# Kernel tuning notes

Hardware: AMD Instinct MI355X
Metric: run time of the kernel (lower is better)

The kernel has to match this reference:

```python
import jax, jax.numpy as jnp
import numpy as np

C = 512
H_HEADS = 8  # self-attn heads (num_heads) and cross-attn heads (n_heads), both 8


def _self_attn(x, Wq, Wkv):
    # x: [B,N,C]; shared (ModuleParallel) linear weights, qkv_bias=False
    B, N, _ = x.shape
    h, d = H_HEADS, C // H_HEADS
    q = (x @ Wq.T).reshape(B, N, h, d).transpose(0, 2, 1, 3)          # [B,h,N,d]
    kv = (x @ Wkv.T).reshape(B, N, 2, h, d).transpose(2, 0, 3, 1, 4)  # [2,B,h,N,d]
    k, v = kv[0], kv[1]
    attn = jax.nn.softmax(jnp.einsum('bhnd,bhmd->bhnm', q, k) * (d ** -0.5), axis=-1)
    y = jnp.einsum('bhnm,bhmd->bhnd', attn, v).transpose(0, 2, 1, 3).reshape(B, N, C)
    return y


def _judger(y_self, y_other, Wj1, bj1, Wj2, bj2):
    # Mlp_2(2C->C->C) with exact GELU, then softmax over channel dim
    hdn = jax.nn.gelu(jnp.concatenate([y_self, y_other], axis=-1) @ Wj1.T + bj1, approximate=False)
    return jax.nn.softmax(hdn @ Wj2.T + bj2, axis=-1)


def _cross_attn(yq, ykv, kn_row, vn_row, Win, bin_, Wout, bout, rel):
    # Vectorized form of the per-sample loop: each token is a seq-len-1 query
    # attending over 2 keys: [noise_k + yq, yq * relation_score].
    B, N, _ = yq.shape
    h, d = H_HEADS, C // H_HEADS
    qw, kw, vw = Win[:C], Win[C:2 * C], Win[2 * C:]
    bq, bk, bv = bin_[:C], bin_[C:2 * C], bin_[2 * C:]
    k_in = jnp.stack([kn_row + yq, yq * rel], axis=-2)   # [B,N,2,C]
    v_in = jnp.stack([vn_row + yq, ykv], axis=-2)        # [B,N,2,C]
    qp = (yq @ qw.T + bq).reshape(B, N, h, d)
    kp = (k_in @ kw.T + bk).reshape(B, N, 2, h, d)
    vp = (v_in @ vw.T + bv).reshape(B, N, 2, h, d)
    scores = jnp.einsum('bnhd,bnkhd->bnhk', qp, kp) * (d ** -0.5)
    w = jax.nn.softmax(scores, axis=-1)
    o = jnp.einsum('bnhk,bnkhd->bnhd', w, vp).reshape(B, N, C)
    return o @ Wout.T + bout


def setup_inputs() -> dict:
    key = jax.random.key(0)
    ks = jax.random.split(key, 16)
    B, N = 8, 1024
    s = 0.02
    inp = {
        'x0': jax.random.normal(ks[0], (B, N, C), jnp.float32),
        'x1': jax.random.normal(ks[1], (B, N, C), jnp.float32),
        'H': 32, 'W': 32,
        'Wq': jax.random.normal(ks[2], (C, C), jnp.float32) * s,
        'Wkv': jax.random.normal(ks[3], (2 * C, C), jnp.float32) * s,
        'Wj1': jax.random.normal(ks[4], (C, 2 * C), jnp.float32) * s,
        'bj1': jnp.zeros((C,), jnp.float32),
        'Wj2': jax.random.normal(ks[5], (C, C), jnp.float32) * s,
        'bj2': jnp.zeros((C,), jnp.float32),
        'kn': jax.random.normal(ks[6], (2, C), jnp.float32),
        'vn': jax.random.normal(ks[7], (2, C), jnp.float32),
        'Wc0_in': jax.random.normal(ks[8], (3 * C, C), jnp.float32) * s,
        'bc0_in': jnp.zeros((3 * C,), jnp.float32),
        'Wc0_out': jax.random.normal(ks[9], (C, C), jnp.float32) * s,
        'bc0_out': jnp.zeros((C,), jnp.float32),
        'Wc1_in': jax.random.normal(ks[10], (3 * C, C), jnp.float32) * s,
        'bc1_in': jnp.zeros((3 * C,), jnp.float32),
        'Wc1_out': jax.random.normal(ks[11], (C, C), jnp.float32) * s,
        'bc1_out': jnp.zeros((C,), jnp.float32),
        'Wp': jax.random.normal(ks[12], (C, C), jnp.float32) * s,
        'bp': jnp.zeros((C,), jnp.float32),
    }
    return inp


def reference(x0, x1, H, W, Wq, Wkv, Wj1, bj1, Wj2, bj2, kn, vn,
              Wc0_in, bc0_in, Wc0_out, bc0_out, Wc1_in, bc1_in, Wc1_out, bc1_out,
              Wp, bp):
    # Dual self-attention (shared q/kv projections across modalities, sr_ratio=1)
    y0 = _self_attn(x0, Wq, Wkv)
    y1 = _self_attn(x1, Wq, Wkv)
    # Noise-augmented relation-gated cross-attention (vectorized over batch)
    rel0 = _judger(y0, y1, Wj1, bj1, Wj2, bj2)
    rel1 = _judger(y1, y0, Wj1, bj1, Wj2, bj2)
    new0 = y0 + _cross_attn(y0, y1, kn[0], vn[0], Wc0_in, bc0_in, Wc0_out, bc0_out, rel0)
    new1 = y1 + _cross_attn(y1, y0, kn[1], vn[1], Wc1_in, bc1_in, Wc1_out, bc1_out, rel1)
    out0 = new0 @ Wp.T + bp
    out1 = new1 @ Wp.T + bp
    return jnp.stack([out0, out1])  # [2,B,N,C]
```

## Files before the change

### kernel.cpp

```cpp
#include <hip/hip_runtime.h>

typedef unsigned short u16;
typedef u16 u16x8 __attribute__((ext_vector_type(8)));
typedef __bf16 bf16x8 __attribute__((ext_vector_type(8)));
typedef __bf16 bf16x2 __attribute__((ext_vector_type(2)));
typedef float f32x4 __attribute__((ext_vector_type(4)));

__device__ __forceinline__ float b2f(u16 h) {
  union { unsigned u; float f; } x; x.u = ((unsigned)h) << 16; return x.f;
}
__device__ __forceinline__ u16 f2b(float f) {
  union { float f; unsigned u; } x; x.f = f;
  unsigned r = x.u + 0x7FFFu + ((x.u >> 16) & 1u);
  return (u16)(r >> 16);
}
__device__ __forceinline__ f32x4 mfma16(bf16x8 a, bf16x8 b, f32x4 c) {
  return __builtin_amdgcn_mfma_f32_16x16x32_bf16(a, b, c, 0, 0, 0);
}
__device__ __forceinline__ void gload16(const void* g, void* l) {
  __builtin_amdgcn_global_load_lds(
      (const __attribute__((address_space(1))) void*)g,
      (__attribute__((address_space(3))) void*)l, 16, 0, 0);
}

__global__ __launch_bounds__(256) void xcvt_k(const float* __restrict__ x0,
                                              const float* __restrict__ x1,
                                              u16* __restrict__ out) {
  int b = blockIdx.x;
  const float* src = (b < 4096) ? x0 : x1;
  u16* dst = out + (b < 4096 ? 0 : 4194304);
  int i = (b & 4095) * 1024 + threadIdx.x * 4;
  float4 v = *(const float4*)&src[i];
  dst[i + 0] = f2b(v.x); dst[i + 1] = f2b(v.y);
  dst[i + 2] = f2b(v.z); dst[i + 3] = f2b(v.w);
}

__global__ __launch_bounds__(256) void wcvt_k(
    const float* __restrict__ wq, const float* __restrict__ wkv,
    const float* __restrict__ wj1, const float* __restrict__ wj2,
    const float* __restrict__ wci0, const float* __restrict__ wco0,
    const float* __restrict__ wci1, const float* __restrict__ wco1,
    const float* __restrict__ wp, u16* __restrict__ wsb) {
  int b = blockIdx.x; const float* src; size_t doff; int lb;
  if      (b < 256)  { src = wq;   doff = 0;       lb = b; }
  else if (b < 768)  { src = wkv;  doff = 262144;  lb = b - 256; }
  else if (b < 1280) { src = wj1;  doff = 786432;  lb = b - 768; }
  else if (b < 1536) { src = wj2;  doff = 1310720; lb = b - 1280; }
  else if (b < 2304) { src = wci0; doff = 1572864; lb = b - 1536; }
  else if (b < 2560) { src = wco0; doff = 2359296; lb = b - 2304; }
  else if (b < 3328) { src = wci1; doff = 2621440; lb = b - 2560; }
  else if (b < 3584) { src = wco1; doff = 3407872; lb = b - 3328; }
  else               { src = wp;   doff = 3670016; lb = b - 3584; }
  int i = lb * 1024 + threadIdx.x * 4;
  float4 v = *(const float4*)&src[i];
  u16* dst = wsb + doff + i;
  dst[0] = f2b(v.x); dst[1] = f2b(v.y); dst[2] = f2b(v.z); dst[3] = f2b(v.w);
}

__global__ __launch_bounds__(256) void cvec_k(const float* __restrict__ kn,
                                              const float* __restrict__ vn,
                                              const u16* __restrict__ wci0,
                                              const u16* __restrict__ wci1,
                                              float* __restrict__ out) {
  int idx = blockIdx.x * 256 + threadIdx.x;
  int which = idx >> 9, col = idx & 511;
  int s = which & 1, isv = which >> 1;
  const float* src = (isv ? vn : kn) + s * 512;
  const u16* w = (s ? wci1 : wci0) + (isv ? 524288 : 262144) + (size_t)col * 512;
  float acc = 0.f;
  for (int k = 0; k < 512; k += 8) {
    u16x8 w8 = *(const u16x8*)&w[k];
#pragma unroll
    for (int j = 0; j < 8; j++) acc += src[k + j] * b2f(w8[j]);
  }
  out[idx] = acc;
}

template<int EPI, int AMODE, bool GLA>
__global__ __launch_bounds__(512, 4) void gemm3_k(
    const u16* __restrict__ A, int K1, int K,
    const u16* __restrict__ W0, const u16* __restrict__ W1,
    const float* __restrict__ b0, const float* __restrict__ b1,
    const u16* __restrict__ mulmat,
    const u16* __restrict__ resid, void* __restrict__ outp, int N) {
  __shared__ u16 SM[32768];
  const int tid = threadIdx.x;
  const int lane = tid & 63;
  const int wv = tid >> 6;
  const int wr = wv >> 1, wc = wv & 1;
  const int lr = lane & 15, lg = lane >> 4;
  const int row0 = blockIdx.x * 128, col0 = blockIdx.y * 128;
  const int strm = (row0 >= 8192) ? 1 : 0;
  const u16* W = strm ? W1 : W0;
  const float* bias = strm ? b1 : b0;
  const int shift = (AMODE == 4 && col0 >= 1536) ? 512 : 0;
  const int cxor  = (AMODE == 4 && col0 >= 1536) ? 8192 : 0;
  const int rL = tid >> 3;
  const int bcl = (lane & 7) * 16;

  f32x4 acc[2][4];
#pragma unroll
  for (int m = 0; m < 2; m++)
#pragma unroll
    for (int n = 0; n < 4; n++) acc[m][n] = f32x4{0.f, 0.f, 0.f, 0.f};

  const int nk = K >> 6;

  auto stage = [&](int k0, int buf) {
    const int Ab = buf * 16384, Wb = buf * 16384 + 8192;
#pragma unroll
    for (int ch = 0; ch < 2; ch++) {
      int r = ch * 64 + rL;
      int bcs = bcl ^ ((r & 7) << 4);
      if constexpr (GLA) {
        const char* asrc;
        if constexpr (AMODE == 3) {
          if (k0 < K1)
            asrc = (const char*)(A + (size_t)(row0 + r) * K1) + k0 * 2 + bcs;
          else
            asrc = (const char*)(A + (size_t)((row0 + r) ^ 8192) * K1) +
                   (k0 - K1) * 2 + bcs;
        } else {
          asrc = (const char*)(A + (size_t)((row0 + r) ^ cxor) * K1) +
                 k0 * 2 + bcs;
        }
        gload16(asrc, &SM[Ab + (ch * 64 + wv * 8) * 64]);
      } else {
        int sc = (lane & 7) * 8;
        int kg = k0 + sc;
        u16x8 v = *(const u16x8*)(A + (size_t)(row0 + r) * K1 + kg);
        if (AMODE == 2) {
          u16x8 m8 = *(const u16x8*)(mulmat + (size_t)(row0 + r) * K1 + kg);
#pragma unroll
          for (int j = 0; j < 8; j++) v[j] = f2b(b2f(v[j]) * b2f(m8[j]));
        }
        *(u16x8*)&SM[Ab + r * 64 + (sc ^ ((r & 7) << 3))] = v;
      }
      const char* wsrc =
          (const char*)(W + (size_t)(col0 - shift + r) * K) + k0 * 2 + bcs;
      gload16(wsrc, &SM[Wb + (ch * 64 + wv * 8) * 64]);
    }
  };

  stage(0, 0);
  __syncthreads();
  for (int t = 0; t < nk; t++) {
    const int buf = t & 1;
    if (t + 1 < nk) stage((t + 1) * 64, buf ^ 1);
    const int Ab = buf * 16384, Wb = buf * 16384 + 8192;
#pragma unroll
    for (int kk = 0; kk < 2; kk++) {
      const int c = kk * 32 + lg * 8;
      bf16x8 af[2], wf[4];
#pragma unroll
      for (int m = 0; m < 2; m++) {
        int r = wr * 32 + m * 16 + lr;
        af[m] = *(const bf16x8*)&SM[Ab + r * 64 + (c ^ ((r & 7) << 3))];
      }
#pragma unroll
      for (int n = 0; n < 4; n++) {
        int r = wc * 64 + n * 16 + lr;
        wf[n] = *(const bf16x8*)&SM[Wb + r * 64 + (c ^ ((r & 7) << 3))];
      }
#pragma unroll
      for (int m = 0; m < 2; m++)
#pragma unroll
        for (int n = 0; n < 4; n++)
          acc[m][n] = mfma16(af[m], wf[n], acc[m][n]);
    }
    __syncthreads();
  }

#pragma unroll
  for (int m = 0; m < 2; m++)
#pragma unroll
    for (int n = 0; n < 4; n++)
#pragma unroll
      for (int r = 0; r < 4; r++) {
        int grow = row0 + wr * 32 + m * 16 + lg * 4 + r;
        int gcol = col0 + wc * 64 + n * 16 + lr;
        float v = acc[m][n][r];
        if (bias) v += bias[gcol - shift];
        if (EPI == 1) v = 0.5f * v * (1.0f + erff(v * 0.70710678118f));
        if (EPI == 2) v += b2f(resid[(size_t)grow * N + gcol]);
        if (EPI == 3) ((float*)outp)[(size_t)grow * N + gcol] = v;
        else          ((u16*)outp)[(size_t)grow * N + gcol] = f2b(v);
      }
}

__global__ __launch_bounds__(256) void vtrans_k(const u16* __restrict__ QKV,
                                                u16* __restrict__ VT) {
  __shared__ u16 t[64][66];
  const int tid = threadIdx.x;
  const int bh = blockIdx.y;
  const int sb = bh >> 3, h = bh & 7;
  const int n0 = blockIdx.x * 64;
#pragma unroll
  for (int i = 0; i < 16; i++) {
    int idx = tid + i * 256;
    int r = idx >> 6, c = idx & 63;
    t[r][c] = QKV[((size_t)sb * 1024 + n0 + r) * 1536 + 1024 + h * 64 + c];
  }
  __syncthreads();
#pragma unroll
  for (int i = 0; i < 16; i++) {
    int idx = tid + i * 256;
    int r = idx >> 6, p = idx & 63;
    int tok = ((p >> 5) << 5) + ((p & 31) >> 1) + ((p & 1) << 4);
    VT[((size_t)bh * 64 + r) * 1024 + n0 + p] = t[tok][r];
  }
}

__global__ __launch_bounds__(256) void attn_k(const u16* __restrict__ QKV,
                                              const u16* __restrict__ VT,
                                              u16* __restrict__ Y) {
  __shared__ u16 SM[24576];
  const int STR = 1536;
  const int tid = threadIdx.x, lane = tid & 63, wv = tid >> 6;
  const int lr = lane & 15, lg = lane >> 4;
  const int L = blockIdx.x;
  const int by = L & 127;
  const int q0 = (L >> 7) * 128;
  const int sb = by >> 3, h = by & 7;
  const size_t rowbase = (size_t)sb * 1024;
  const int bcl = (lane & 7) * 16;
  const float SC = 0.18033688f;

  bf16x8 qa[2][2];
#pragma unroll
  for (int m = 0; m < 2; m++)
#pragma unroll
    for (int kk = 0; kk < 2; kk++) {
      int r = q0 + wv * 32 + m * 16 + lr;
      int c = h * 64 + kk * 32 + lg * 8;
      qa[m][kk] = *(const bf16x8*)&QKV[(rowbase + r) * STR + c];
    }

  f32x4 o[2][4];
#pragma unroll
  for (int m = 0; m < 2; m++)
#pragma unroll
    for (int n = 0; n < 4; n++) o[m][n] = f32x4{0.f, 0.f, 0.f, 0.f};
  float ls[2][4] = {{0.f, 0.f, 0.f, 0.f}, {0.f, 0.f, 0.f, 0.f}};

  auto stagekv = [&](int c0, int buf) {
#pragma unroll
    for (int ch = 0; ch < 2; ch++) {
      int r = ch * 32 + (tid >> 3);
      int bcs = bcl ^ ((r & 7) << 4);
      const char* ks =
          (const char*)(QKV + (rowbase + c0 + r) * STR + 512 + h * 64) + bcs;
      gload16(ks, &SM[buf * 8192 + (ch * 32 + wv * 8) * 64]);
      const char* vs =
          (const char*)(VT + ((size_t)by * 64 + r) * 1024 + c0) + bcs;
      gload16(vs, &SM[buf * 8192 + 4096 + (ch * 32 + wv * 8) * 64]);
    }
  };

  stagekv(0, 0);
  __syncthreads();
  for (int t = 0; t < 16; t++) {
    const int buf = t & 1;
    if (t < 15) stagekv((t + 1) * 64, buf ^ 1);
    const int Kb = buf * 8192, Vb = buf * 8192 + 4096;

    f32x4 s[2][4];
#pragma unroll
    for (int m = 0; m < 2; m++)
#pragma unroll
      for (int n = 0; n < 4; n++) s[m][n] = f32x4{0.f, 0.f, 0.f, 0.f};
#pragma unroll
    for (int kk = 0; kk < 2; kk++) {
      const int c = kk * 32 + lg * 8;
      bf16x8 kf[4];
#pragma unroll
      for (int n = 0; n < 4; n++) {
        int r = n * 16 + lr;
        kf[n] = *(const bf16x8*)&SM[Kb + r * 64 + (c ^ ((r & 7) << 3))];
      }
#pragma unroll
      for (int m = 0; m < 2; m++)
#pragma unroll
        for (int n = 0; n < 4; n++) s[m][n] = mfma16(qa[m][kk], kf[n], s[m][n]);
    }
#pragma unroll
    for (int m = 0; m < 2; m++)
#pragma unroll
      for (int r = 0; r < 4; r++) {
        int prow = wv * 32 + m * 16 + lg * 4 + r;
        float p00 = __builtin_amdgcn_exp2f(s[m][0][r] * SC);
        float p01 = __builtin_amdgcn_exp2f(s[m][1][r] * SC);
        float p10 = __builtin_amdgcn_exp2f(s[m][2][r] * SC);
        float p11 = __builtin_amdgcn_exp2f(s[m][3][r] * SC);
        ls[m][r] += (p00 + p01) + (p10 + p11);
        bf16x2 w0; w0[0] = (__bf16)p00; w0[1] = (__bf16)p01;
        bf16x2 w1; w1[0] = (__bf16)p10; w1[1] = (__bf16)p11;
        int ib = 16384 + prow * 64, xr = (prow & 7) << 3;
        *(bf16x2*)&SM[ib + ((lr * 2) ^ xr)] = w0;
        *(bf16x2*)&SM[ib + ((32 + lr * 2) ^ xr)] = w1;
      }
#pragma unroll
    for (int kc = 0; kc < 2; kc++) {
      const int cc = kc * 32 + lg * 8;
      bf16x8 pa[2], vf[4];
#pragma unroll
      for (int m = 0; m < 2; m++) {
        int r = wv * 32 + m * 16 + lr;
        pa[m] = *(const bf16x8*)&SM[16384 + r * 64 + (cc ^ ((r & 7) << 3))];
      }
#pragma unroll
      for (int n = 0; n < 4; n++) {
        int r = n * 16 + lr;
        vf[n] = *(const bf16x8*)&SM[Vb + r * 64 + (cc ^ ((r & 7) << 3))];
      }
#pragma unroll
      for (int m = 0; m < 2; m++)
#pragma unroll
        for (int n = 0; n < 4; n++) o[m][n] = mfma16(pa[m], vf[n], o[m][n]);
    }
    __syncthreads();
  }

#pragma unroll
  for (int m = 0; m < 2; m++)
#pragma unroll
    for (int r = 0; r < 4; r++) {
      float v = ls[m][r];
      v += __shfl_xor(v, 1); v += __shfl_xor(v, 2);
      v += __shfl_xor(v, 4); v += __shfl_xor(v, 8);
      ls[m][r] = v;
    }
#pragma unroll
  for (int m = 0; m < 2; m++)
#pragma unroll
    for (int n = 0; n < 4; n++)
#pragma unroll
      for (int r = 0; r < 4; r++) {
        int grow = q0 + wv * 32 + m * 16 + lg * 4 + r;
        int gcol = h * 64 + n * 16 + lr;
        Y[(rowbase + grow) * 512 + gcol] = f2b(o[m][n][r] / ls[m][r]);
      }
}

__global__ __launch_bounds__(256) void rsoftmax_k(u16* __restrict__ X) {
  const int row = blockIdx.x * 4 + (threadIdx.x >> 6);
  const int lane = threadIdx.x & 63;
  u16* p = X + (size_t)row * 512 + lane * 8;
  u16x8 v = *(u16x8*)p;
  float e[8]; float s = 0.f;
#pragma unroll
  for (int j = 0; j < 8; j++) { e[j] = __expf(b2f(v[j])); s += e[j]; }
  for (int x = 1; x < 64; x <<= 1) s += __shfl_xor(s, x);
  float inv = 1.0f / s;
#pragma unroll
  for (int j = 0; j < 8; j++) v[j] = f2b(e[j] * inv);
  *(u16x8*)p = v;
}

__global__ __launch_bounds__(256) void twokey3_k(const u16* __restrict__ CP,
                                                 const u16* __restrict__ KP1,
                                                 const float* __restrict__ cvec,
                                                 u16* __restrict__ o) {
  const int t = blockIdx.x * 4 + (threadIdx.x >> 6);
  const int lane = threadIdx.x & 63;
  const int s = t >> 13;
  const size_t rb = (size_t)t * 2048 + lane * 8;
  u16x8 q8 = *(const u16x8*)&CP[rb];
  u16x8 a8 = *(const u16x8*)&CP[rb + 512];
  u16x8 v0 = *(const u16x8*)&CP[rb + 1024];
  u16x8 v1 = *(const u16x8*)&CP[rb + 1536];
  u16x8 b8 = *(const u16x8*)&KP1[(size_t)t * 512 + lane * 8];
  const float* ck = cvec + s * 512 + lane * 8;
  const float* cv = cvec + 1024 + s * 512 + lane * 8;

  float s0 = 0.f, s1 = 0.f;
#pragma unroll
  for (int j = 0; j < 8; j++) {
    float qf = b2f(q8[j]);
    s0 += qf * (b2f(a8[j]) + ck[j]);
    s1 += qf * b2f(b8[j]);
  }
  s0 += __shfl_xor(s0, 1); s1 += __shfl_xor(s1, 1);
  s0 += __shfl_xor(s0, 2); s1 += __shfl_xor(s1, 2);
  s0 += __shfl_xor(s0, 4); s1 += __shfl_xor(s1, 4);

  float e0 = __expf(s0 * 0.125f), e1 = __expf(s1 * 0.125f);
  float rr = 1.0f / (e0 + e1);
  float w0 = e0 * rr, w1 = e1 * rr;
  u16x8 o8;
#pragma unroll
  for (int j = 0; j < 8; j++)
    o8[j] = f2b(w0 * (b2f(v0[j]) + cv[j]) + w1 * b2f(v1[j]));
  *(u16x8*)&o[(size_t)t * 512 + lane * 8] = o8;
}

extern "C" void kernel_launch(void* const* d_in, const int* in_sizes, int n_in,
                              void* d_out, int out_size, void* d_ws, size_t ws_size,
                              hipStream_t stream) {
  (void)in_sizes; (void)n_in; (void)out_size; (void)ws_size;
  const float* x0  = (const float*)d_in[0];
  const float* x1  = (const float*)d_in[1];
  const float* Wq  = (const float*)d_in[4];
  const float* Wkv = (const float*)d_in[5];
  const float* Wj1 = (const float*)d_in[6];
  const float* bj1 = (const float*)d_in[7];
  const float* Wj2 = (const float*)d_in[8];
  const float* bj2 = (const float*)d_in[9];
  const float* kn  = (const float*)d_in[10];
  const float* vn  = (const float*)d_in[11];
  const float* Wci[2]  = {(const float*)d_in[12], (const float*)d_in[16]};
  const float* bci[2]  = {(const float*)d_in[13], (const float*)d_in[17]};
  const float* Wco[2]  = {(const float*)d_in[14], (const float*)d_in[18]};
  const float* bco[2]  = {(const float*)d_in[15], (const float*)d_in[19]};
  const float* Wp  = (const float*)d_in[20];
  const float* bp  = (const float*)d_in[21];

  u16* wsb = (u16*)d_ws;
  u16* wqb  = wsb;
  u16* wj1b = wsb + 786432;
  u16* wj2b = wsb + 1310720;
  u16* wcib[2] = {wsb + 1572864, wsb + 2621440};
  u16* wcob[2] = {wsb + 2359296, wsb + 3407872};
  u16* wpb  = wsb + 3670016;
  float* cvecb = (float*)(wsb + 3932160);
  const size_t SLOT = 8388608;
  u16* base = wsb + 4194304;
  u16* S0 = base;
  u16* S1 = base + 1 * SLOT;
  u16* S2 = base + 2 * SLOT;
  u16* S5 = base + 5 * SLOT;
  u16* S6 = base + 6 * SLOT;
  u16* S7 = base + 7 * SLOT;
  u16* QKV = S2;
  u16* CP  = S2;
  u16* REL = S0;

  dim3 blk(256), gblk(512);
  xcvt_k<<<dim3(8192), blk, 0, stream>>>(x0, x1, S0);
  wcvt_k<<<dim3(3840), blk, 0, stream>>>(Wq, Wkv, Wj1, Wj2, Wci[0], Wco[0],
                                         Wci[1], Wco[1], Wp, wsb);
  cvec_k<<<dim3(8), blk, 0, stream>>>(kn, vn, wcib[0], wcib[1], cvecb);

  gemm3_k<0, 0, true><<<dim3(128, 12), gblk, 0, stream>>>(
      S0, 512, 512, wqb, wqb, nullptr, nullptr, nullptr, nullptr, QKV, 1536);
  vtrans_k<<<dim3(16, 128), blk, 0, stream>>>(QKV, S5);
  attn_k<<<dim3(1024), blk, 0, stream>>>(QKV, S5, S1);

  gemm3_k<1, 3, true><<<dim3(128, 4), gblk, 0, stream>>>(
      S1, 512, 1024, wj1b, wj1b, bj1, bj1, nullptr, nullptr, S2, 512);
  gemm3_k<0, 0, true><<<dim3(128, 4), gblk, 0, stream>>>(
      S2, 512, 512, wj2b, wj2b, bj2, bj2, nullptr, nullptr, REL, 512);
  rsoftmax_k<<<dim3(4096), blk, 0, stream>>>(REL);

  gemm3_k<0, 2, false><<<dim3(128, 4), gblk, 0, stream>>>(
      S1, 512, 512, wcib[0] + 262144, wcib[1] + 262144,
      bci[0] + 512, bci[1] + 512, REL, nullptr, S6, 512);
  gemm3_k<0, 4, true><<<dim3(128, 16), gblk, 0, stream>>>(
      S1, 512, 512, wcib[0], wcib[1], bci[0], bci[1], nullptr, nullptr,
      CP, 2048);

  twokey3_k<<<dim3(4096), blk, 0, stream>>>(CP, S6, cvecb, S7);

  gemm3_k<2, 0, true><<<dim3(128, 4), gblk, 0, stream>>>(
      S7, 512, 512, wcob[0], wcob[1], bco[0], bco[1], nullptr, S1, S0, 512);
  gemm3_k<3, 0, true><<<dim3(128, 4), gblk, 0, stream>>>(
      S0, 512, 512, wpb, wpb, bp, bp, nullptr, nullptr, d_out, 512);
}
```

Before: 321.8 us.

## Fold cross-attn output projection into final projection and tune GEMM scheduling

Precomputes the product Wp·Wco per stream and folds the residual and biases into one K=1024 GEMM over a concatenated [y | attn_out] buffer. This removes one full 8192x2-row GEMM pass and its intermediate round trip. It also adds an XCD-aware 1D block-to-tile mapping and replaces __syncthreads with explicit vmcnt/lgkmcnt waits so the next stage's loads stay in flight. The composed weight product is rounded to bf16, which adds some numerical error.

```diff
diff --git a/kernel.cpp b/kernel.cpp
--- a/kernel.cpp
+++ b/kernel.cpp
@@ -22,6 +22,10 @@
       (const __attribute__((address_space(1))) void*)g,
       (__attribute__((address_space(3))) void*)l, 16, 0, 0);
 }
+#define WAITV4 asm volatile("s_waitcnt vmcnt(4)" ::: "memory")
+#define WAITV0 asm volatile("s_waitcnt vmcnt(0)" ::: "memory")
+#define WAITL0 asm volatile("s_waitcnt lgkmcnt(0)" ::: "memory")
+#define BARRIER asm volatile("s_barrier" ::: "memory")
 
 __global__ __launch_bounds__(256) void xcvt_k(const float* __restrict__ x0,
                                               const float* __restrict__ x1,
@@ -38,8 +42,7 @@
 __global__ __launch_bounds__(256) void wcvt_k(
     const float* __restrict__ wq, const float* __restrict__ wkv,
     const float* __restrict__ wj1, const float* __restrict__ wj2,
-    const float* __restrict__ wci0, const float* __restrict__ wco0,
-    const float* __restrict__ wci1, const float* __restrict__ wco1,
+    const float* __restrict__ wci0, const float* __restrict__ wci1,
     const float* __restrict__ wp, u16* __restrict__ wsb) {
   int b = blockIdx.x; const float* src; size_t doff; int lb;
   if      (b < 256)  { src = wq;   doff = 0;       lb = b; }
@@ -47,27 +50,67 @@
   else if (b < 1280) { src = wj1;  doff = 786432;  lb = b - 768; }
   else if (b < 1536) { src = wj2;  doff = 1310720; lb = b - 1280; }
   else if (b < 2304) { src = wci0; doff = 1572864; lb = b - 1536; }
-  else if (b < 2560) { src = wco0; doff = 2359296; lb = b - 2304; }
-  else if (b < 3328) { src = wci1; doff = 2621440; lb = b - 2560; }
-  else if (b < 3584) { src = wco1; doff = 3407872; lb = b - 3328; }
-  else               { src = wp;   doff = 3670016; lb = b - 3584; }
+  else if (b < 3072) { src = wci1; doff = 2359296; lb = b - 2304; }
+  else               { src = wp;   doff = 3145728; lb = b - 3072; }
   int i = lb * 1024 + threadIdx.x * 4;
   float4 v = *(const float4*)&src[i];
   u16* dst = wsb + doff + i;
-  dst[0] = f2b(v.x); dst[1] = f2b(v.y); dst[2] = f2b(v.z); dst[3] = f2b(v.w);
-}
-
-__global__ __launch_bounds__(256) void cvec_k(const float* __restrict__ kn,
-                                              const float* __restrict__ vn,
-                                              const u16* __restrict__ wci0,
-                                              const u16* __restrict__ wci1,
-                                              float* __restrict__ out) {
+  u16 c0 = f2b(v.x), c1 = f2b(v.y), c2 = f2b(v.z), c3 = f2b(v.w);
+  dst[0] = c0; dst[1] = c1; dst[2] = c2; dst[3] = c3;
+  if (b >= 3072) {
+    int row = i >> 9, col = i & 511;
+    u16* f0 = wsb + 3932160 + (size_t)row * 1024 + col;
+    u16* f1 = wsb + 4456448 + (size_t)row * 1024 + col;
+    f0[0] = c0; f0[1] = c1; f0[2] = c2; f0[3] = c3;
+    f1[0] = c0; f1[1] = c1; f1[2] = c2; f1[3] = c3;
+  }
+}
+
+__global__ __launch_bounds__(256) void tcvt_k(const float* __restrict__ w0,
+                                              const float* __restrict__ w1,
+                                              u16* __restrict__ o0,
+                                              u16* __restrict__ o1) {
+  __shared__ u16 t[64][65];
+  const int b = blockIdx.x;
+  const float* src = (b & 64) ? w1 : w0;
+  u16* dst = (b & 64) ? o1 : o0;
+  const int r0 = ((b >> 3) & 7) * 64, c0 = (b & 7) * 64;
+  const int tid = threadIdx.x;
+#pragma unroll
+  for (int i = 0; i < 16; i++) {
+    int idx = tid + i * 256;
+    int r = idx >> 6, c = idx & 63;
+    t[r][c] = f2b(src[(size_t)(r0 + r) * 512 + c0 + c]);
+  }
+  __syncthreads();
+#pragma unroll
+  for (int i = 0; i < 16; i++) {
+    int idx = tid + i * 256;
+    int c = idx >> 6, r = idx & 63;
+    dst[(size_t)(c0 + c) * 512 + r0 + r] = t[r][c];
+  }
+}
+
+__global__ __launch_bounds__(256) void cvec_k(
+    const float* __restrict__ kn, const float* __restrict__ vn,
+    const float* __restrict__ bp, const float* __restrict__ bco0,
+    const float* __restrict__ bco1, const u16* __restrict__ wci0,
+    const u16* __restrict__ wci1, const u16* __restrict__ wp,
+    float* __restrict__ out) {
   int idx = blockIdx.x * 256 + threadIdx.x;
   int which = idx >> 9, col = idx & 511;
-  int s = which & 1, isv = which >> 1;
-  const float* src = (isv ? vn : kn) + s * 512;
-  const u16* w = (s ? wci1 : wci0) + (isv ? 524288 : 262144) + (size_t)col * 512;
-  float acc = 0.f;
+  const float* src; const u16* w; float acc;
+  if (which < 4) {
+    int s = which & 1, isv = which >> 1;
+    src = (isv ? vn : kn) + s * 512;
+    w = (s ? wci1 : wci0) + (isv ? 524288 : 262144) + (size_t)col * 512;
+    acc = 0.f;
+  } else {
+    int s = which & 1;
+    src = s ? bco1 : bco0;
+    w = wp + (size_t)col * 512;
+    acc = bp[col];
+  }
   for (int k = 0; k < 512; k += 8) {
     u16x8 w8 = *(const u16x8*)&w[k];
 #pragma unroll
@@ -77,19 +120,27 @@
 }
 
 template<int EPI, int AMODE, bool GLA>
-__global__ __launch_bounds__(512, 4) void gemm3_k(
-    const u16* __restrict__ A, int K1, int K,
+__global__ __launch_bounds__(512, 4) void gemm4_k(
+    const u16* __restrict__ A, int astr, int K1, int K,
     const u16* __restrict__ W0, const u16* __restrict__ W1,
     const float* __restrict__ b0, const float* __restrict__ b1,
     const u16* __restrict__ mulmat,
-    const u16* __restrict__ resid, void* __restrict__ outp, int N) {
+    void* __restrict__ outp, int ostr, int ncol) {
   __shared__ u16 SM[32768];
   const int tid = threadIdx.x;
   const int lane = tid & 63;
   const int wv = tid >> 6;
   const int wr = wv >> 1, wc = wv & 1;
   const int lr = lane & 15, lg = lane >> 4;
-  const int row0 = blockIdx.x * 128, col0 = blockIdx.y * 128;
+  const int L = blockIdx.x;
+  const int nrow = gridDim.x / ncol;
+  int row_b, col_b;
+  if ((nrow & 7) == 0) {
+    int xcd = L & 7, s = L >> 3;
+    row_b = xcd * (nrow >> 3) + s / ncol;
+    col_b = s % ncol;
+  } else { row_b = L % nrow; col_b = L / nrow; }
+  const int row0 = row_b * 128, col0 = col_b * 128;
   const int strm = (row0 >= 8192) ? 1 : 0;
   const u16* W = strm ? W1 : W0;
   const float* bias = strm ? b1 : b0;
@@ -116,21 +167,21 @@
         const char* asrc;
         if constexpr (AMODE == 3) {
           if (k0 < K1)
-            asrc = (const char*)(A + (size_t)(row0 + r) * K1) + k0 * 2 + bcs;
+            asrc = (const char*)(A + (size_t)(row0 + r) * astr) + k0 * 2 + bcs;
           else
-            asrc = (const char*)(A + (size_t)((row0 + r) ^ 8192) * K1) +
+            asrc = (const char*)(A + (size_t)((row0 + r) ^ 8192) * astr) +
                    (k0 - K1) * 2 + bcs;
         } else {
-          asrc = (const char*)(A + (size_t)((row0 + r) ^ cxor) * K1) +
+          asrc = (const char*)(A + (size_t)((row0 + r) ^ cxor) * astr) +
                  k0 * 2 + bcs;
         }
         gload16(asrc, &SM[Ab + (ch * 64 + wv * 8) * 64]);
       } else {
         int sc = (lane & 7) * 8;
         int kg = k0 + sc;
-        u16x8 v = *(const u16x8*)(A + (size_t)(row0 + r) * K1 + kg);
+        u16x8 v = *(const u16x8*)(A + (size_t)(row0 + r) * astr + kg);
         if (AMODE == 2) {
-          u16x8 m8 = *(const u16x8*)(mulmat + (size_t)(row0 + r) * K1 + kg);
+          u16x8 m8 = *(const u16x8*)(mulmat + (size_t)(row0 + r) * K + kg);
 #pragma unroll
           for (int j = 0; j < 8; j++) v[j] = f2b(b2f(v[j]) * b2f(m8[j]));
         }
@@ -143,10 +194,15 @@
   };
 
   stage(0, 0);
-  __syncthreads();
   for (int t = 0; t < nk; t++) {
     const int buf = t & 1;
-    if (t + 1 < nk) stage((t + 1) * 64, buf ^ 1);
+    if (t + 1 < nk) {
+      stage((t + 1) * 64, buf ^ 1);
+      if (GLA && AMODE != 2) { WAITV4; } else { WAITV0; }
+    } else {
+      WAITV0;
+    }
+    BARRIER;
     const int Ab = buf * 16384, Wb = buf * 16384 + 8192;
 #pragma unroll
     for (int kk = 0; kk < 2; kk++) {
@@ -168,7 +224,8 @@
         for (int n = 0; n < 4; n++)
           acc[m][n] = mfma16(af[m], wf[n], acc[m][n]);
     }
-    __syncthreads();
+    WAITL0;
+    BARRIER;
   }
 
 #pragma unroll
@@ -182,9 +239,8 @@
         float v = acc[m][n][r];
         if (bias) v += bias[gcol - shift];
         if (EPI == 1) v = 0.5f * v * (1.0f + erff(v * 0.70710678118f));
-        if (EPI == 2) v += b2f(resid[(size_t)grow * N + gcol]);
-        if (EPI == 3) ((float*)outp)[(size_t)grow * N + gcol] = v;
-        else          ((u16*)outp)[(size_t)grow * N + gcol] = f2b(v);
+        if (EPI == 3) ((float*)outp)[(size_t)grow * ostr + gcol] = v;
+        else          ((u16*)outp)[(size_t)grow * ostr + gcol] = f2b(v);
       }
 }
 
@@ -213,7 +269,7 @@
 
 __global__ __launch_bounds__(256) void attn_k(const u16* __restrict__ QKV,
                                               const u16* __restrict__ VT,
-                                              u16* __restrict__ Y) {
+                                              u16* __restrict__ OC) {
   __shared__ u16 SM[24576];
   const int STR = 1536;
   const int tid = threadIdx.x, lane = tid & 63, wv = tid >> 6;
@@ -258,10 +314,15 @@
   };
 
   stagekv(0, 0);
-  __syncthreads();
   for (int t = 0; t < 16; t++) {
     const int buf = t & 1;
-    if (t < 15) stagekv((t + 1) * 64, buf ^ 1);
+    if (t < 15) {
+      stagekv((t + 1) * 64, buf ^ 1);
+      WAITV4;
+    } else {
+      WAITV0;
+    }
+    BARRIER;
     const int Kb = buf * 8192, Vb = buf * 8192 + 4096;
 
     f32x4 s[2][4];
@@ -318,7 +379,8 @@
 #pragma unroll
         for (int n = 0; n < 4; n++) o[m][n] = mfma16(pa[m], vf[n], o[m][n]);
     }
-    __syncthreads();
+    WAITL0;
+    BARRIER;
   }
 
 #pragma unroll
@@ -338,7 +400,7 @@
       for (int r = 0; r < 4; r++) {
         int grow = q0 + wv * 32 + m * 16 + lg * 4 + r;
         int gcol = h * 64 + n * 16 + lr;
-        Y[(rowbase + grow) * 512 + gcol] = f2b(o[m][n][r] / ls[m][r]);
+        OC[(rowbase + grow) * 1024 + gcol] = f2b(o[m][n][r] / ls[m][r]);
       }
 }
 
@@ -360,7 +422,7 @@
 __global__ __launch_bounds__(256) void twokey3_k(const u16* __restrict__ CP,
                                                  const u16* __restrict__ KP1,
                                                  const float* __restrict__ cvec,
-                                                 u16* __restrict__ o) {
+                                                 u16* __restrict__ OC) {
   const int t = blockIdx.x * 4 + (threadIdx.x >> 6);
   const int lane = threadIdx.x & 63;
   const int s = t >> 13;
@@ -391,7 +453,7 @@
 #pragma unroll
   for (int j = 0; j < 8; j++)
     o8[j] = f2b(w0 * (b2f(v0[j]) + cv[j]) + w1 * b2f(v1[j]));
-  *(u16x8*)&o[(size_t)t * 512 + lane * 8] = o8;
+  *(u16x8*)&OC[(size_t)t * 1024 + 512 + lane * 8] = o8;
 }
 
 extern "C" void kernel_launch(void* const* d_in, const int* in_sizes, int n_in,
@@ -416,53 +478,60 @@
   const float* bp  = (const float*)d_in[21];
 
   u16* wsb = (u16*)d_ws;
-  u16* wqb  = wsb;
-  u16* wj1b = wsb + 786432;
-  u16* wj2b = wsb + 1310720;
-  u16* wcib[2] = {wsb + 1572864, wsb + 2621440};
-  u16* wcob[2] = {wsb + 2359296, wsb + 3407872};
-  u16* wpb  = wsb + 3670016;
-  float* cvecb = (float*)(wsb + 3932160);
+  u16* wqb   = wsb;
+  u16* wj1b  = wsb + 786432;
+  u16* wj2b  = wsb + 1310720;
+  u16* wcib[2] = {wsb + 1572864, wsb + 2359296};
+  u16* wpb   = wsb + 3145728;
+  u16* wcoT[2] = {wsb + 3407872, wsb + 3670016};
+  u16* wfin[2] = {wsb + 3932160, wsb + 4456448};
+  float* cvecb = (float*)(wsb + 4980736);
   const size_t SLOT = 8388608;
-  u16* base = wsb + 4194304;
+  u16* base = wsb + 5242880;
   u16* S0 = base;
-  u16* S1 = base + 1 * SLOT;
-  u16* S2 = base + 2 * SLOT;
+  u16* OC = base + 1 * SLOT;
+  u16* S3 = base + 3 * SLOT;
+  u16* S4 = base + 4 * SLOT;
   u16* S5 = base + 5 * SLOT;
   u16* S6 = base + 6 * SLOT;
-  u16* S7 = base + 7 * SLOT;
-  u16* QKV = S2;
-  u16* CP  = S2;
-  u16* REL = S0;
+  u16* QKV = S3;
+  u16* REL = S3;
+  u16* CP  = S3;
+  (void)S4; (void)S5;
 
   dim3 blk(256), gblk(512);
   xcvt_k<<<dim3(8192), blk, 0, stream>>>(x0, x1, S0);
-  wcvt_k<<<dim3(3840), blk, 0, stream>>>(Wq, Wkv, Wj1, Wj2, Wci[0], Wco[0],
-                                         Wci[1], Wco[1], Wp, wsb);
-  cvec_k<<<dim3(8), blk, 0, stream>>>(kn, vn, wcib[0], wcib[1], cvecb);
-
-  gemm3_k<0, 0, true><<<dim3(128, 12), gblk, 0, stream>>>(
-      S0, 512, 512, wqb, wqb, nullptr, nullptr, nullptr, nullptr, QKV, 1536);
-  vtrans_k<<<dim3(16, 128), blk, 0, stream>>>(QKV, S5);
-  attn_k<<<dim3(1024), blk, 0, stream>>>(QKV, S5, S1);
-
-  gemm3_k<1, 3, true><<<dim3(128, 4), gblk, 0, stream>>>(
-      S1, 512, 1024, wj1b, wj1b, bj1, bj1, nullptr, nullptr, S2, 512);
-  gemm3_k<0, 0, true><<<dim3(128, 4), gblk, 0, stream>>>(
-      S2, 512, 512, wj2b, wj2b, bj2, bj2, nullptr, nullptr, REL, 512);
+  wcvt_k<<<dim3(3328), blk, 0, stream>>>(Wq, Wkv, Wj1, Wj2, Wci[0], Wci[1],
+                                         Wp, wsb);
+  tcvt_k<<<dim3(128), blk, 0, stream>>>(Wco[0], Wco[1], wcoT[0], wcoT[1]);
+  cvec_k<<<dim3(12), blk, 0, stream>>>(kn, vn, bp, bco[0], bco[1],
+                                       wcib[0], wcib[1], wpb, cvecb);
+  for (int s = 0; s < 2; s++)
+    gemm4_k<0, 0, true><<<dim3(16), gblk, 0, stream>>>(
+        wpb, 512, 512, 512, wcoT[s], wcoT[s], nullptr, nullptr, nullptr,
+        wfin[s] + 512, 1024, 4);
+
+  gemm4_k<0, 0, true><<<dim3(1536), gblk, 0, stream>>>(
+      S0, 512, 512, 512, wqb, wqb, nullptr, nullptr, nullptr, QKV, 1536, 12);
+  vtrans_k<<<dim3(16, 128), blk, 0, stream>>>(QKV, S6);
+  attn_k<<<dim3(1024), blk, 0, stream>>>(QKV, S6, OC);
+
+  gemm4_k<1, 3, true><<<dim3(512), gblk, 0, stream>>>(
+      OC, 1024, 512, 1024, wj1b, wj1b, bj1, bj1, nullptr, S0, 512, 4);
+  gemm4_k<0, 0, true><<<dim3(512), gblk, 0, stream>>>(
+      S0, 512, 512, 512, wj2b, wj2b, bj2, bj2, nullptr, REL, 512, 4);
   rsoftmax_k<<<dim3(4096), blk, 0, stream>>>(REL);
 
-  gemm3_k<0, 2, false><<<dim3(128, 4), gblk, 0, stream>>>(
-      S1, 512, 512, wcib[0] + 262144, wcib[1] + 262144,
-      bci[0] + 512, bci[1] + 512, REL, nullptr, S6, 512);
-  gemm3_k<0, 4, true><<<dim3(128, 16), gblk, 0, stream>>>(
-      S1, 512, 512, wcib[0], wcib[1], bci[0], bci[1], nullptr, nullptr,
-      CP, 2048);
-
-  twokey3_k<<<dim3(4096), blk, 0, stream>>>(CP, S6, cvecb, S7);
-
-  gemm3_k<2, 0, true><<<dim3(128, 4), gblk, 0, stream>>>(
-      S7, 512, 512, wcob[0], wcob[1], bco[0], bco[1], nullptr, S1, S0, 512);
-  gemm3_k<3, 0, true><<<dim3(128, 4), gblk, 0, stream>>>(
-      S0, 512, 512, wpb, wpb, bp, bp, nullptr, nullptr, d_out, 512);
-}
+  gemm4_k<0, 2, false><<<dim3(512), gblk, 0, stream>>>(
+      OC, 1024, 512, 512, wcib[0] + 262144, wcib[1] + 262144,
+      bci[0] + 512, bci[1] + 512, REL, S0, 512, 4);
+  gemm4_k<0, 4, true><<<dim3(2048), gblk, 0, stream>>>(
+      OC, 1024, 512, 512, wcib[0], wcib[1], bci[0], bci[1], nullptr,
+      CP, 2048, 16);
+
+  twokey3_k<<<dim3(4096), blk, 0, stream>>>(CP, S0, cvecb, OC);
+
+  gemm4_k<3, 0, true><<<dim3(512), gblk, 0, stream>>>(
+      OC, 1024, 1024, 1024, wfin[0], wfin[1], cvecb + 2048, cvecb + 2560,
+      nullptr, d_out, 512, 4);
+}
```

After: 316.5 us. No clear change (-1.6%).
